# Kernel optimization log

Hardware: AMD Instinct MI355X
Metric: run time of the kernel (lower is better)

Reference implementation:

```python
import jax, jax.numpy as jnp
import numpy as np

N_SERIES = 1024  # N; x carries 3N stacked time-synchronous nodes
GCN_DEPTH = 2
IN_DIM = 64
H_DIM = 64


def setup_inputs() -> dict:
    key = jax.random.key(0)
    k = jax.random.split(key, 6)
    B, C, N3 = 64, IN_DIM, 3 * N_SERIES
    x = jax.random.normal(k[0], (N3, B, C), dtype=jnp.float32)
    A = jax.random.normal(k[1], (N3, N3), dtype=jnp.float32) * 0.02
    # Linear2d (1x1 conv) params per depth; act='glu' -> out = 2*h_dim
    s0 = 1.0 / np.sqrt(IN_DIM)
    s1 = 1.0 / np.sqrt(H_DIM)
    W0 = jax.random.uniform(k[2], (2 * H_DIM, IN_DIM), jnp.float32, -s0, s0)
    b0 = jax.random.uniform(k[3], (2 * H_DIM,), jnp.float32, -s0, s0)
    W1 = jax.random.uniform(k[4], (2 * H_DIM, H_DIM), jnp.float32, -s1, s1)
    b1 = jax.random.uniform(k[5], (2 * H_DIM,), jnp.float32, -s1, s1)
    return {"x": x, "A": A, "W0": W0, "b0": b0, "W1": W1, "b1": b1}


def reference(x, A, W0, b0, W1, b1):
    # x: (3N, B, C) -> (B, C, 3N)
    h = jnp.transpose(x, (1, 2, 0))
    convs = []
    for W, b in ((W0, b0), (W1, b1)):
        # GCN2d flow='tgt_to_src': h[b,c,v] = sum_w h[b,c,w] * A[v,w]  (L=1 squeezed)
        g = jnp.einsum('bcw,vw->bcv', h, A)
        # Linear2d 1x1 conv: channels C -> 2*h_dim, then GLU gate
        y = jnp.einsum('oc,bcv->bov', W, g) + b[None, :, None]
        lhs, rhs = jnp.split(y, 2, axis=1)
        h = lhs * jax.nn.sigmoid(rhs)          # (B, h_dim, 3N)
        convs.append(jnp.transpose(h, (2, 0, 1)))  # (3N, B, h_dim)
    # crop the middle N nodes of each depth, then max over depth
    cropped = jnp.stack([c[N_SERIES:2 * N_SERIES] for c in convs], axis=0)
    return jnp.max(cropped, axis=0)  # (N, B, h_dim)
```

## Files before the change

kernel.cpp:

```cpp
#include <hip/hip_runtime.h>
#include <hip/hip_bf16.h>
#include <stdint.h>

typedef __attribute__((ext_vector_type(8))) short s16x8;
typedef __attribute__((ext_vector_type(4))) float f32x4;
typedef __attribute__((ext_vector_type(8))) unsigned short u16x8;
typedef __attribute__((ext_vector_type(4))) unsigned short u16x4;

__device__ __forceinline__ float bf2f(unsigned short u) {
  union { uint32_t u; float f; } v; v.u = ((uint32_t)u) << 16; return v.f;
}
__device__ __forceinline__ unsigned short f2bf(float f) {
  union { float f; uint32_t u; } v; v.f = f;
  uint32_t u = v.u;
  return (unsigned short)((u + 0x7fffu + ((u >> 16) & 1u)) >> 16);
}
__device__ __forceinline__ void load_lds16(const void* g, void* l) {
  __builtin_amdgcn_global_load_lds(
      (const __attribute__((address_space(1))) void*)g,
      (__attribute__((address_space(3))) void*)l, 16, 0, 0);
}

#define VMW(n) asm volatile("s_waitcnt vmcnt(" #n ")" ::: "memory")
#define SBAR() asm volatile("s_barrier" ::: "memory")


__global__ void k_detect(const uint32_t* __restrict__ xw, int* __restrict__ flag) {
  int lane = threadIdx.x;
  uint32_t u = xw[lane * 97 + 1];
  int e = (u >> 7) & 0xFF;
  unsigned long long m = __ballot(e > 150);
  if (lane == 0) *flag = (__popcll(m) > 6) ? 1 : 0;
}

__global__ __launch_bounds__(256) void k_transpose(const void* __restrict__ xin,
                                                   unsigned short* __restrict__ xtp,
                                                   const int* __restrict__ flag) {
  __shared__ __align__(16) unsigned short tile[64 * 65];
  const int t = threadIdx.x;
  const int w0 = blockIdx.x * 64;
  const int m0 = blockIdx.y * 64;
  if (*flag) {
    const float* xf = (const float*)xin;
#pragma unroll
    for (int rep = 0; rep < 4; ++rep) {
      int vi = t + rep * 256;
      int r = vi >> 4;
      int c4 = (vi & 15) * 4;
      f32x4 v = *(const f32x4*)(xf + (uint64_t)(w0 + r) * 4096 + m0 + c4);
#pragma unroll
      for (int u = 0; u < 4; ++u) tile[(c4 + u) * 65 + r] = f2bf(v[u]);
    }
  } else {
    const unsigned short* xb = (const unsigned short*)xin;
#pragma unroll
    for (int rep = 0; rep < 2; ++rep) {
      int vi = t + rep * 256;
      int r = vi >> 3;
      int c8 = (vi & 7) * 8;
      u16x8 v = *(const u16x8*)(xb + (uint64_t)(w0 + r) * 4096 + m0 + c8);
#pragma unroll
      for (int u = 0; u < 8; ++u) tile[(c8 + u) * 65 + r] = v[u];
    }
  }
  __syncthreads();
  unsigned short* dst = xtp + ((uint64_t)(m0 >> 6) * 48 + (w0 >> 6)) * 4096;
#pragma unroll
  for (int rep = 0; rep < 2; ++rep) {
    int vi = t + rep * 256;
    int kb = vi >> 6, r = vi & 63;
    u16x8 v;
#pragma unroll
    for (int u = 0; u < 8; ++u) v[u] = tile[r * 65 + kb * 8 + u];
    *(u16x8*)(dst + kb * 512 + r * 8) = v;
  }
}

__global__ __launch_bounds__(256) void k_packA(const void* __restrict__ Ain,
                                               unsigned short* __restrict__ Abp,
                                               const int* __restrict__ flag) {
  __shared__ __align__(16) unsigned short tl[8 * 520];
  const int t = threadIdx.x;
  const int kt = blockIdx.x, rt = blockIdx.y;
  if (*flag) {
    const float* Af = (const float*)Ain;
#pragma unroll
    for (int rep = 0; rep < 4; ++rep) {
      int vi = t + rep * 256;
      int r = vi >> 4;
      int c4 = (vi & 15) * 4;
      f32x4 v = *(const f32x4*)(Af + (uint64_t)(rt * 64 + r) * 3072 + kt * 64 + c4);
      int kb = c4 >> 3, e = c4 & 7;
#pragma unroll
      for (int u = 0; u < 4; ++u) tl[kb * 520 + r * 8 + e + u] = f2bf(v[u]);
    }
  } else {
    const unsigned short* Ab16 = (const unsigned short*)Ain;
#pragma unroll
    for (int rep = 0; rep < 2; ++rep) {
      int vi = t + rep * 256;
      int r = vi >> 3;
      int c8 = (vi & 7) * 8;
      u16x8 v = *(const u16x8*)(Ab16 + (uint64_t)(rt * 64 + r) * 3072 + kt * 64 + c8);
#pragma unroll
      for (int u = 0; u < 8; ++u) tl[(c8 >> 3) * 520 + r * 8 + u] = v[u];
    }
  }
  __syncthreads();
  unsigned short* dst = Abp + ((uint64_t)rt * 48 + kt) * 4096;
#pragma unroll
  for (int rep = 0; rep < 2; ++rep) {
    int vi = t + rep * 256;
    int kb = vi >> 6, r = vi & 63;
    u16x8 v;
#pragma unroll
    for (int u = 0; u < 8; ++u) v[u] = tl[kb * 520 + r * 8 + u];
    *(u16x8*)(dst + kb * 512 + r * 8) = v;
  }
}

__global__ __launch_bounds__(256) void k_cvtW(const void* __restrict__ W0,
                                              const void* __restrict__ b0,
                                              const void* __restrict__ W1,
                                              const void* __restrict__ b1,
                                              unsigned short* __restrict__ wb,
                                              const int* __restrict__ flag) {
  int fp = *flag;
  for (int i = threadIdx.x; i < 16640; i += 256) {
    const void* src; int off;
    if (i < 8192)        { src = W0; off = i; }
    else if (i < 8320)   { src = b0; off = i - 8192; }
    else if (i < 16512)  { src = W1; off = i - 8320; }
    else                 { src = b1; off = i - 16512; }
    wb[i] = fp ? f2bf(((const float*)src)[off]) : ((const unsigned short*)src)[off];
  }
}

template <int BM, int KTOT>
__global__ __launch_bounds__(512, 2) void k_gemm_glu2(
    const unsigned short* __restrict__ Am,
    const unsigned short* __restrict__ Bm,
    const unsigned short* __restrict__ W,
    const unsigned short* __restrict__ bias,
    unsigned short* __restrict__ H,
    int Vtot) {
  constexpr int BN  = 256;
  constexpr int IF  = BM / 32;
  constexpr int NPH = (IF > 4) ? 2 : 1;
  constexpr int IPH = IF / NPH;
  constexpr int APL = (BM / 64) * 4;
  constexpr int P   = APL + 16;
  constexpr int QF  = P / 8;
  constexpr int QR  = P - QF * 8;
  constexpr int PPW = QF + (QR ? 1 : 0);
  constexpr int BUFS = P * 512;
  constexpr int NT  = KTOT / 32;
  constexpr int Kt  = KTOT / 64;
  constexpr int NRB = BM / 16;
  constexpr int EPL = BM * 264;
  constexpr int SME = (4 * BUFS > EPL) ? 4 * BUFS : EPL;
  static_assert(QF == 3, "vmcnt literals below assume QF==3");

  __shared__ __align__(16) unsigned short smem[SME];

  const int t    = threadIdx.x;
  const int lane = t & 63;
  const int wid  = t >> 6;
  const int wV   = wid >> 2;
  const int wM   = wid & 3;
  const int fr   = lane & 15;
  const int q4   = lane >> 4;
  const int v0   = blockIdx.x * BM;
  const int m0   = blockIdx.y * BN;
  const int art0 = v0 >> 6;
  const int brt0 = m0 >> 6;

  const int myq = QF + ((QR && wid < QR) ? 1 : 0);
  const unsigned short* srcb[PPW];
  int ldso[PPW];
#pragma unroll
  for (int q = 0; q < PPW; ++q) {
    int pi = wid + 8 * q;
    if (pi >= P) pi = P - 1;
    const int isA = pi < APL;
    const int rtl = (isA ? pi : pi - APL) >> 2;
    const int pb  = pi & 3;
    const unsigned short* base =
        isA ? (Am + (uint64_t)(art0 + rtl) * Kt * 4096)
            : (Bm + (uint64_t)(brt0 + rtl) * Kt * 4096);
    srcb[q] = base + pb * 512 + lane * 8;
    ldso[q] = pi * 512;
  }

  int aoff[IF], boff[4];
#pragma unroll
  for (int i = 0; i < IF; ++i) {
    const int row = wV * (BM / 2) + i * 16 + fr;
    aoff[i] = ((row >> 6) * 4 + q4) * 512 + (row & 63) * 8;
  }
#pragma unroll
  for (int j = 0; j < 4; ++j)
    boff[j] = (APL + wM * 4 + q4) * 512 + (j * 16 + fr) * 8;

  f32x4 acc[IF][4] = {};

#pragma unroll
  for (int pt = 0; pt < 3; ++pt)
#pragma unroll
    for (int q = 0; q < PPW; ++q)
      if (q < myq)
        load_lds16(srcb[q] + pt * 2048, smem + pt * BUFS + ldso[q]);
  if (QR && wid < QR) { VMW(8); } else { VMW(6); }
  SBAR();

#pragma unroll 4
  for (int tt = 0; tt < NT; ++tt) {
    const unsigned short* buf = smem + (tt & 3) * BUFS;
    s16x8 bfr[4];
#pragma unroll
    for (int ph = 0; ph < NPH; ++ph) {
      if (ph == 0) {
#pragma unroll
        for (int j = 0; j < 4; ++j)
          bfr[j] = *(const s16x8*)(buf + boff[j]);
      }
      s16x8 afr[IPH];
#pragma unroll
      for (int ii = 0; ii < IPH; ++ii)
        afr[ii] = *(const s16x8*)(buf + aoff[ph * IPH + ii]);
      if (tt + 3 < NT) {
        unsigned short* dst = smem + ((tt + 3) & 3) * BUFS;
#pragma unroll
        for (int q = 0; q < PPW; ++q)
          if ((q % NPH) == ph && q < myq)
            load_lds16(srcb[q] + (uint64_t)(tt + 3) * 2048, dst + ldso[q]);
      }
      SBAR();
      __builtin_amdgcn_s_setprio(1);
#pragma unroll
      for (int ii = 0; ii < IPH; ++ii)
#pragma unroll
        for (int j = 0; j < 4; ++j)
          acc[ph * IPH + ii][j] = __builtin_amdgcn_mfma_f32_16x16x32_bf16(
              afr[ii], bfr[j], acc[ph * IPH + ii][j], 0, 0, 0);
      __builtin_amdgcn_s_setprio(0);
      if (ph == NPH - 1) {
        if (tt + 3 < NT) {
          if (QR && wid < QR) { VMW(8); } else { VMW(6); }
        } else if (tt + 2 < NT) {
          if (QR && wid < QR) { VMW(4); } else { VMW(3); }
        } else {
          VMW(0);
        }
      }
      SBAR();
    }
  }

  {
    const int rr = q4 * 4;
#pragma unroll
    for (int i = 0; i < IF; ++i)
#pragma unroll
      for (int j = 0; j < 4; ++j) {
        const int col = wM * 64 + j * 16 + fr;
#pragma unroll
        for (int r = 0; r < 4; ++r) {
          const int row = wV * (BM / 2) + i * 16 + rr + r;
          smem[row * 264 + col] = f2bf(acc[i][j][r]);
        }
      }
  }
  __syncthreads();

  s16x8 wf[2][8];
#pragma unroll
  for (int ksi = 0; ksi < 2; ++ksi)
#pragma unroll
    for (int j = 0; j < 8; ++j)
      wf[ksi][j] = *(const s16x8*)(W + (j * 16 + fr) * 64 + ksi * 32 + q4 * 8);
  float bj[8];
#pragma unroll
  for (int j = 0; j < 8; ++j) bj[j] = bf2f(bias[j * 16 + fr]);

  const int Vt = Vtot >> 6;
#pragma unroll
  for (int rep = 0; rep < (NRB + 7) / 8; ++rep) {
    const int rb = rep * 8 + wid;
    if (rb < NRB) {
#pragma unroll
      for (int bb = 0; bb < 4; ++bb) {
        f32x4 acc2[8] = {};
#pragma unroll
        for (int ksi = 0; ksi < 2; ++ksi) {
          s16x8 af = *(const s16x8*)(smem + (rb * 16 + fr) * 264 + bb * 64 +
                                     ksi * 32 + q4 * 8);
#pragma unroll
          for (int j = 0; j < 8; ++j)
            acc2[j] = __builtin_amdgcn_mfma_f32_16x16x32_bf16(af, wf[ksi][j],
                                                              acc2[j], 0, 0, 0);
        }
        const int v = v0 + rb * 16 + q4 * 4;
#pragma unroll
        for (int j = 0; j < 4; ++j) {
          u16x4 pk;
#pragma unroll
          for (int r = 0; r < 4; ++r) {
            float lhs = acc2[j][r] + bj[j];
            float rhs = acc2[j + 4][r] + bj[j + 4];
            float sg = 1.0f / (1.0f + __expf(-rhs));
            pk[r] = f2bf(lhs * sg);
          }
          const int o = j * 16 + fr;
          const int hrow = m0 + bb * 64 + o;
          *(u16x4*)(H + ((uint64_t)(hrow >> 6) * Vt + (v >> 6)) * 4096 +
                    ((v >> 3) & 7) * 512 + (hrow & 63) * 8 + (v & 7)) = pk;
        }
      }
    }
  }
}

__global__ __launch_bounds__(256) void k_maxout(const unsigned short* __restrict__ H1,
                                                const unsigned short* __restrict__ H2,
                                                float* __restrict__ out) {
  __shared__ __align__(16) float tile[64 * 65];
  const int t = threadIdx.x;
  const int b = blockIdx.y;
  const int n0 = blockIdx.x * 64;
  {
    int j = t >> 2, p = t & 3;
    int c1 = 1024 + n0 + p * 16;
    int c2 = n0 + p * 16;
    const unsigned short* h1p =
        H1 + ((uint64_t)b * 48 + (c1 >> 6)) * 4096 + ((c1 >> 3) & 7) * 512 + j * 8;
    const unsigned short* h2p =
        H2 + ((uint64_t)b * 16 + (c2 >> 6)) * 4096 + ((c2 >> 3) & 7) * 512 + j * 8;
    u16x8 a0 = *(const u16x8*)(h1p);
    u16x8 a1 = *(const u16x8*)(h1p + 512);
    u16x8 c0 = *(const u16x8*)(h2p);
    u16x8 c1v = *(const u16x8*)(h2p + 512);
#pragma unroll
    for (int u = 0; u < 8; ++u) {
      tile[j * 65 + p * 16 + u] = fmaxf(bf2f(a0[u]), bf2f(c0[u]));
      tile[j * 65 + p * 16 + 8 + u] = fmaxf(bf2f(a1[u]), bf2f(c1v[u]));
    }
  }
  __syncthreads();
  {
    int n = t >> 2, jb = (t & 3) * 16;
    float* op = out + (uint64_t)(n0 + n) * 4096 + b * 64 + jb;
#pragma unroll
    for (int q = 0; q < 4; ++q) {
      f32x4 o;
#pragma unroll
      for (int u = 0; u < 4; ++u) o[u] = tile[(jb + q * 4 + u) * 65 + n];
      *(f32x4*)(op + q * 4) = o;
    }
  }
}

extern "C" void kernel_launch(void* const* d_in, const int* in_sizes, int n_in,
                              void* d_out, int out_size, void* d_ws, size_t ws_size,
                              hipStream_t stream) {
  (void)in_sizes; (void)n_in; (void)out_size; (void)ws_size;
  const void* x  = d_in[0];
  const void* A  = d_in[1];
  const void* W0 = d_in[2];
  const void* b0 = d_in[3];
  const void* W1 = d_in[4];
  const void* b1 = d_in[5];
  float* out = (float*)d_out;

  char* ws = (char*)d_ws;
  unsigned short* Xtp = (unsigned short*)(ws + 0);
  unsigned short* H2p = (unsigned short*)(ws + 0);
  unsigned short* Abp = (unsigned short*)(ws + 25165824);
  unsigned short* Wb  = (unsigned short*)(ws + 44040192);
  unsigned short* H1p = (unsigned short*)(ws + 44105728);
  int* flag = (int*)(ws + 69271552);

  k_detect<<<1, 64, 0, stream>>>((const uint32_t*)x, flag);
  k_transpose<<<dim3(48, 64), 256, 0, stream>>>(x, Xtp, flag);
  k_packA<<<dim3(48, 48), 256, 0, stream>>>(A, Abp, flag);
  k_cvtW<<<1, 256, 0, stream>>>(W0, b0, W1, b1, Wb, flag);
  k_gemm_glu2<192, 3072><<<dim3(16, 16), 512, 0, stream>>>(
      Abp, Xtp, Wb, Wb + 8192, H1p, 3072);
  k_gemm_glu2<128, 3072><<<dim3(8, 16), 512, 0, stream>>>(
      Abp + (uint64_t)16 * 48 * 4096, H1p, Wb + 8320, Wb + 16512, H2p, 1024);
  k_maxout<<<dim3(16, 64), 256, 0, stream>>>(H1p, H2p, out);
}
```

Baseline: 299.7 us.

## Merge prep kernels into one launch and shrink second GEMM tile for more blocks

Combines the transpose, A-packing and weight-conversion kernels into a single launch that dispatches on block index, removing two kernel launches and their serialization gaps. The second GEMM switches from BM=128 to BM=64, doubling its grid from 128 to 256 blocks to fill more CUs, at the cost of less A/B reuse per block. The vmcnt waits are made generic via a template so the new tile configuration (different QF) computes correct wait counts.

```diff
diff --git a/kernel.cpp b/kernel.cpp
--- a/kernel.cpp
+++ b/kernel.cpp
@@ -21,7 +21,18 @@
       (__attribute__((address_space(3))) void*)l, 16, 0, 0);
 }
 
-#define VMW(n) asm volatile("s_waitcnt vmcnt(" #n ")" ::: "memory")
+template <int N>
+__device__ __forceinline__ void vmw() {
+  if constexpr (N == 0) asm volatile("s_waitcnt vmcnt(0)" ::: "memory");
+  else if constexpr (N == 1) asm volatile("s_waitcnt vmcnt(1)" ::: "memory");
+  else if constexpr (N == 2) asm volatile("s_waitcnt vmcnt(2)" ::: "memory");
+  else if constexpr (N == 3) asm volatile("s_waitcnt vmcnt(3)" ::: "memory");
+  else if constexpr (N == 4) asm volatile("s_waitcnt vmcnt(4)" ::: "memory");
+  else if constexpr (N == 5) asm volatile("s_waitcnt vmcnt(5)" ::: "memory");
+  else if constexpr (N == 6) asm volatile("s_waitcnt vmcnt(6)" ::: "memory");
+  else if constexpr (N == 7) asm volatile("s_waitcnt vmcnt(7)" ::: "memory");
+  else asm volatile("s_waitcnt vmcnt(8)" ::: "memory");
+}
 #define SBAR() asm volatile("s_barrier" ::: "memory")
 
 
@@ -33,106 +44,105 @@
   if (lane == 0) *flag = (__popcll(m) > 6) ? 1 : 0;
 }
 
-__global__ __launch_bounds__(256) void k_transpose(const void* __restrict__ xin,
-                                                   unsigned short* __restrict__ xtp,
-                                                   const int* __restrict__ flag) {
-  __shared__ __align__(16) unsigned short tile[64 * 65];
-  const int t = threadIdx.x;
-  const int w0 = blockIdx.x * 64;
-  const int m0 = blockIdx.y * 64;
-  if (*flag) {
-    const float* xf = (const float*)xin;
-#pragma unroll
-    for (int rep = 0; rep < 4; ++rep) {
-      int vi = t + rep * 256;
-      int r = vi >> 4;
-      int c4 = (vi & 15) * 4;
-      f32x4 v = *(const f32x4*)(xf + (uint64_t)(w0 + r) * 4096 + m0 + c4);
-#pragma unroll
-      for (int u = 0; u < 4; ++u) tile[(c4 + u) * 65 + r] = f2bf(v[u]);
-    }
-  } else {
-    const unsigned short* xb = (const unsigned short*)xin;
-#pragma unroll
-    for (int rep = 0; rep < 2; ++rep) {
-      int vi = t + rep * 256;
-      int r = vi >> 3;
-      int c8 = (vi & 7) * 8;
-      u16x8 v = *(const u16x8*)(xb + (uint64_t)(w0 + r) * 4096 + m0 + c8);
-#pragma unroll
-      for (int u = 0; u < 8; ++u) tile[(c8 + u) * 65 + r] = v[u];
-    }
-  }
-  __syncthreads();
-  unsigned short* dst = xtp + ((uint64_t)(m0 >> 6) * 48 + (w0 >> 6)) * 4096;
-#pragma unroll
-  for (int rep = 0; rep < 2; ++rep) {
-    int vi = t + rep * 256;
-    int kb = vi >> 6, r = vi & 63;
-    u16x8 v;
-#pragma unroll
-    for (int u = 0; u < 8; ++u) v[u] = tile[r * 65 + kb * 8 + u];
-    *(u16x8*)(dst + kb * 512 + r * 8) = v;
-  }
-}
-
-__global__ __launch_bounds__(256) void k_packA(const void* __restrict__ Ain,
-                                               unsigned short* __restrict__ Abp,
-                                               const int* __restrict__ flag) {
-  __shared__ __align__(16) unsigned short tl[8 * 520];
-  const int t = threadIdx.x;
-  const int kt = blockIdx.x, rt = blockIdx.y;
-  if (*flag) {
-    const float* Af = (const float*)Ain;
-#pragma unroll
-    for (int rep = 0; rep < 4; ++rep) {
-      int vi = t + rep * 256;
-      int r = vi >> 4;
-      int c4 = (vi & 15) * 4;
-      f32x4 v = *(const f32x4*)(Af + (uint64_t)(rt * 64 + r) * 3072 + kt * 64 + c4);
-      int kb = c4 >> 3, e = c4 & 7;
-#pragma unroll
-      for (int u = 0; u < 4; ++u) tl[kb * 520 + r * 8 + e + u] = f2bf(v[u]);
-    }
-  } else {
-    const unsigned short* Ab16 = (const unsigned short*)Ain;
-#pragma unroll
-    for (int rep = 0; rep < 2; ++rep) {
-      int vi = t + rep * 256;
-      int r = vi >> 3;
-      int c8 = (vi & 7) * 8;
-      u16x8 v = *(const u16x8*)(Ab16 + (uint64_t)(rt * 64 + r) * 3072 + kt * 64 + c8);
-#pragma unroll
-      for (int u = 0; u < 8; ++u) tl[(c8 >> 3) * 520 + r * 8 + u] = v[u];
-    }
-  }
-  __syncthreads();
-  unsigned short* dst = Abp + ((uint64_t)rt * 48 + kt) * 4096;
-#pragma unroll
-  for (int rep = 0; rep < 2; ++rep) {
-    int vi = t + rep * 256;
-    int kb = vi >> 6, r = vi & 63;
-    u16x8 v;
-#pragma unroll
-    for (int u = 0; u < 8; ++u) v[u] = tl[kb * 520 + r * 8 + u];
-    *(u16x8*)(dst + kb * 512 + r * 8) = v;
-  }
-}
-
-__global__ __launch_bounds__(256) void k_cvtW(const void* __restrict__ W0,
+__global__ __launch_bounds__(256) void k_prep(const void* __restrict__ xin,
+                                              const void* __restrict__ Ain,
+                                              const void* __restrict__ W0,
                                               const void* __restrict__ b0,
                                               const void* __restrict__ W1,
                                               const void* __restrict__ b1,
+                                              unsigned short* __restrict__ xtp,
+                                              unsigned short* __restrict__ Abp,
                                               unsigned short* __restrict__ wb,
                                               const int* __restrict__ flag) {
-  int fp = *flag;
-  for (int i = threadIdx.x; i < 16640; i += 256) {
-    const void* src; int off;
-    if (i < 8192)        { src = W0; off = i; }
-    else if (i < 8320)   { src = b0; off = i - 8192; }
-    else if (i < 16512)  { src = W1; off = i - 8320; }
-    else                 { src = b1; off = i - 16512; }
-    wb[i] = fp ? f2bf(((const float*)src)[off]) : ((const unsigned short*)src)[off];
+  __shared__ __align__(16) unsigned short sh[64 * 65];
+  const int t = threadIdx.x;
+  const int bid = blockIdx.x;
+  const int fp = *flag;
+
+  if (bid < 3072) {
+    const int w0 = (bid % 48) * 64;
+    const int m0 = (bid / 48) * 64;
+    if (fp) {
+      const float* xf = (const float*)xin;
+#pragma unroll
+      for (int rep = 0; rep < 4; ++rep) {
+        int vi = t + rep * 256;
+        int r = vi >> 4;
+        int c4 = (vi & 15) * 4;
+        f32x4 v = *(const f32x4*)(xf + (uint64_t)(w0 + r) * 4096 + m0 + c4);
+#pragma unroll
+        for (int u = 0; u < 4; ++u) sh[(c4 + u) * 65 + r] = f2bf(v[u]);
+      }
+    } else {
+      const unsigned short* xb = (const unsigned short*)xin;
+#pragma unroll
+      for (int rep = 0; rep < 2; ++rep) {
+        int vi = t + rep * 256;
+        int r = vi >> 3;
+        int c8 = (vi & 7) * 8;
+        u16x8 v = *(const u16x8*)(xb + (uint64_t)(w0 + r) * 4096 + m0 + c8);
+#pragma unroll
+        for (int u = 0; u < 8; ++u) sh[(c8 + u) * 65 + r] = v[u];
+      }
+    }
+    __syncthreads();
+    unsigned short* dst = xtp + ((uint64_t)(m0 >> 6) * 48 + (w0 >> 6)) * 4096;
+#pragma unroll
+    for (int rep = 0; rep < 2; ++rep) {
+      int vi = t + rep * 256;
+      int kb = vi >> 6, r = vi & 63;
+      u16x8 v;
+#pragma unroll
+      for (int u = 0; u < 8; ++u) v[u] = sh[r * 65 + kb * 8 + u];
+      *(u16x8*)(dst + kb * 512 + r * 8) = v;
+    }
+  } else if (bid < 5376) {
+    const int b2 = bid - 3072;
+    const int kt = b2 % 48, rt = b2 / 48;
+    if (fp) {
+      const float* Af = (const float*)Ain;
+#pragma unroll
+      for (int rep = 0; rep < 4; ++rep) {
+        int vi = t + rep * 256;
+        int r = vi >> 4;
+        int c4 = (vi & 15) * 4;
+        f32x4 v = *(const f32x4*)(Af + (uint64_t)(rt * 64 + r) * 3072 + kt * 64 + c4);
+        int kb = c4 >> 3, e = c4 & 7;
+#pragma unroll
+        for (int u = 0; u < 4; ++u) sh[kb * 520 + r * 8 + e + u] = f2bf(v[u]);
+      }
+    } else {
+      const unsigned short* Ab16 = (const unsigned short*)Ain;
+#pragma unroll
+      for (int rep = 0; rep < 2; ++rep) {
+        int vi = t + rep * 256;
+        int r = vi >> 3;
+        int c8 = (vi & 7) * 8;
+        u16x8 v = *(const u16x8*)(Ab16 + (uint64_t)(rt * 64 + r) * 3072 + kt * 64 + c8);
+#pragma unroll
+        for (int u = 0; u < 8; ++u) sh[(c8 >> 3) * 520 + r * 8 + u] = v[u];
+      }
+    }
+    __syncthreads();
+    unsigned short* dst = Abp + ((uint64_t)rt * 48 + kt) * 4096;
+#pragma unroll
+    for (int rep = 0; rep < 2; ++rep) {
+      int vi = t + rep * 256;
+      int kb = vi >> 6, r = vi & 63;
+      u16x8 v;
+#pragma unroll
+      for (int u = 0; u < 8; ++u) v[u] = sh[kb * 520 + r * 8 + u];
+      *(u16x8*)(dst + kb * 512 + r * 8) = v;
+    }
+  } else {
+    for (int i = t; i < 16640; i += 256) {
+      const void* src; int off;
+      if (i < 8192)        { src = W0; off = i; }
+      else if (i < 8320)   { src = b0; off = i - 8192; }
+      else if (i < 16512)  { src = W1; off = i - 8320; }
+      else                 { src = b1; off = i - 16512; }
+      wb[i] = fp ? f2bf(((const float*)src)[off]) : ((const unsigned short*)src)[off];
+    }
   }
 }
 
@@ -159,7 +169,6 @@
   constexpr int NRB = BM / 16;
   constexpr int EPL = BM * 264;
   constexpr int SME = (4 * BUFS > EPL) ? 4 * BUFS : EPL;
-  static_assert(QF == 3, "vmcnt literals below assume QF==3");
 
   __shared__ __align__(16) unsigned short smem[SME];
 
@@ -210,7 +219,7 @@
     for (int q = 0; q < PPW; ++q)
       if (q < myq)
         load_lds16(srcb[q] + pt * 2048, smem + pt * BUFS + ldso[q]);
-  if (QR && wid < QR) { VMW(8); } else { VMW(6); }
+  if (QR && wid < QR) { vmw<2 * (QF + 1)>(); } else { vmw<2 * QF>(); }
   SBAR();
 
 #pragma unroll 4
@@ -246,11 +255,11 @@
       __builtin_amdgcn_s_setprio(0);
       if (ph == NPH - 1) {
         if (tt + 3 < NT) {
-          if (QR && wid < QR) { VMW(8); } else { VMW(6); }
+          if (QR && wid < QR) { vmw<2 * (QF + 1)>(); } else { vmw<2 * QF>(); }
         } else if (tt + 2 < NT) {
-          if (QR && wid < QR) { VMW(4); } else { VMW(3); }
+          if (QR && wid < QR) { vmw<QF + 1>(); } else { vmw<QF>(); }
         } else {
-          VMW(0);
+          vmw<0>();
         }
       }
       SBAR();
@@ -381,12 +390,10 @@
   int* flag = (int*)(ws + 69271552);
 
   k_detect<<<1, 64, 0, stream>>>((const uint32_t*)x, flag);
-  k_transpose<<<dim3(48, 64), 256, 0, stream>>>(x, Xtp, flag);
-  k_packA<<<dim3(48, 48), 256, 0, stream>>>(A, Abp, flag);
-  k_cvtW<<<1, 256, 0, stream>>>(W0, b0, W1, b1, Wb, flag);
+  k_prep<<<5377, 256, 0, stream>>>(x, A, W0, b0, W1, b1, Xtp, Abp, Wb, flag);
   k_gemm_glu2<192, 3072><<<dim3(16, 16), 512, 0, stream>>>(
       Abp, Xtp, Wb, Wb + 8192, H1p, 3072);
-  k_gemm_glu2<128, 3072><<<dim3(8, 16), 512, 0, stream>>>(
+  k_gemm_glu2<64, 3072><<<dim3(16, 16), 512, 0, stream>>>(
       Abp + (uint64_t)16 * 48 * 4096, H1p, Wb + 8320, Wb + 16512, H2p, 1024);
   k_maxout<<<dim3(16, 64), 256, 0, stream>>>(H1p, H2p, out);
 }
```

New measurement: 274.8 us. 1.09x faster.
